# Optimization experiments

Measured on AMD Instinct MI355X. Metric: run time of the kernel, lower is better.

## Reference

```python
import jax, jax.numpy as jnp
import numpy as np

T, D, E, K = 16384, 2048, 128, 8

def setup_inputs() -> dict:
    key = jax.random.key(0)
    k1, k2 = jax.random.split(key)
    hidden_states = jax.random.normal(k1, (T, D), dtype=jnp.float32)
    weight = jax.random.normal(k2, (E, D), dtype=jnp.float32) * 0.02
    return {"hidden_states": hidden_states, "weight": weight}

def reference(hidden_states, weight):
    # (T, D) @ (D, E) -> (T, E) router logits
    x = hidden_states.reshape(-1, weight.shape[1])
    logits = jnp.einsum('td,ed->te', x, weight)
    # softmax in float32 over experts
    router_logits = jax.nn.softmax(logits.astype(jnp.float32), axis=-1)
    # top-k selection + renormalization so selected weights sum to 1
    router_weights, router_indices = jax.lax.top_k(router_logits, K)
    router_weights = router_weights / jnp.sum(router_weights, axis=-1, keepdims=True)
    return (router_logits, router_weights, router_indices)
```

## Files before the change

### kernel.cpp

```cpp
#include <hip/hip_runtime.h>
#include <math.h>


constexpr int T = 16384;
constexpr int D = 2048;
constexpr int E = 128;
constexpr int K = 8;

constexpr int BM = 32;
constexpr int NS = 5;
constexpr int NB = D / 64;

typedef int i32x4 __attribute__((ext_vector_type(4)));

#define MFI8(A, B, C) C = __builtin_amdgcn_mfma_i32_16x16x64_i8(A, B, C, 0, 0, 0)

__device__ __forceinline__ void slice5(float x, float c, float ic, int out[NS]) {
    float r = x;
#pragma unroll
    for (int s = 0; s < NS; ++s) {
        float q = rintf(r * c);
        out[s] = (int)q;
        r = fmaf(q, -ic, r);
        c *= 128.f;
        ic *= (1.f / 128.f);
    }
}

__global__ __launch_bounds__(256)
void w_slice(const float* __restrict__ W, signed char* __restrict__ Ws)
{
    const int e  = blockIdx.x >> 1;
    const int k0 = ((blockIdx.x & 1) << 10) | (threadIdx.x << 2);
    float4 v = *(const float4*)(W + (size_t)e * D + k0);
    int b0[NS], b1[NS], b2[NS], b3[NS];
    slice5(v.x, 512.f, 1.f / 512.f, b0);
    slice5(v.y, 512.f, 1.f / 512.f, b1);
    slice5(v.z, 512.f, 1.f / 512.f, b2);
    slice5(v.w, 512.f, 1.f / 512.f, b3);
#pragma unroll
    for (int s = 0; s < NS; ++s) {
        unsigned lo = __builtin_amdgcn_perm((unsigned)b1[s], (unsigned)b0[s], 0x00000400u);
        unsigned hi = __builtin_amdgcn_perm((unsigned)b3[s], (unsigned)b2[s], 0x00000400u);
        unsigned pk = __builtin_amdgcn_perm(hi, lo, 0x05040100u);
        *(int*)(Ws + (size_t)s * E * D + (size_t)e * D + k0) = (int)pk;
    }
}

__global__ __launch_bounds__(512, 4)
void router_fused(const float* __restrict__ X,
                  const signed char* __restrict__ Ws,
                  float* __restrict__ out)
{
    __shared__ __align__(16) signed char As[2][NS][2][4][16][16];
    __shared__ double Ld[BM][E];

    const int tid = threadIdx.x;
    const long t0 = (long)blockIdx.x * BM;

    const int ar = tid >> 4;
    const int ac = (tid & 15) << 2;
    const float* Xp = X + (t0 + ar) * (long)D + ac;

    const int l  = tid & 63;
    const int wv = tid >> 6;
    const int er = l & 15;
    const int kg = l >> 4;

    const signed char* Wp = Ws + (size_t)(wv * 16 + er) * D + (size_t)kg * 16;

    i32x4 p00 = {}, p01 = {}, p02 = {}, p03 = {}, p04 = {};
    i32x4 p10 = {}, p11 = {}, p12 = {}, p13 = {}, p14 = {};

    auto stage = [&](const float4& v, int buf) {
        int q0[NS], q1[NS], q2[NS], q3[NS];
        slice5(v.x, 16.f, 1.f / 16.f, q0);
        slice5(v.y, 16.f, 1.f / 16.f, q1);
        slice5(v.z, 16.f, 1.f / 16.f, q2);
        slice5(v.w, 16.f, 1.f / 16.f, q3);
        int* dst = (int*)&As[buf][0][ar >> 4][ac >> 4][ar & 15][ac & 15];
#pragma unroll
        for (int s = 0; s < NS; ++s) {
            unsigned lo = __builtin_amdgcn_perm((unsigned)q1[s], (unsigned)q0[s], 0x00000400u);
            unsigned hi = __builtin_amdgcn_perm((unsigned)q3[s], (unsigned)q2[s], 0x00000400u);
            unsigned pk = __builtin_amdgcn_perm(hi, lo, 0x05040100u);
            dst[s * 512] = (int)pk;
        }
    };

    auto tileStep = [&](int buf, int tl,
                        const i32x4& b0, const i32x4& b1, const i32x4& b2,
                        const i32x4& b3, const i32x4& b4,
                        i32x4& d0, i32x4& d1, i32x4& d2, i32x4& d3, i32x4& d4) {
        const signed char* ap = &As[buf][0][tl][0][0][0] + l * 16;
        i32x4 a0 = *(const i32x4*)(ap);
        i32x4 a1 = *(const i32x4*)(ap + 2048);
        i32x4 a2 = *(const i32x4*)(ap + 4096);
        i32x4 a3 = *(const i32x4*)(ap + 6144);
        i32x4 a4 = *(const i32x4*)(ap + 8192);
        MFI8(a0, b0, d0);
        MFI8(a0, b1, d1); MFI8(a1, b0, d1);
        MFI8(a0, b2, d2); MFI8(a1, b1, d2); MFI8(a2, b0, d2);
        MFI8(a0, b3, d3); MFI8(a1, b2, d3); MFI8(a2, b1, d3); MFI8(a3, b0, d3);
        MFI8(a0, b4, d4); MFI8(a1, b3, d4); MFI8(a2, b2, d4); MFI8(a3, b1, d4);
        MFI8(a4, b0, d4);
    };

    float4 xv = *(const float4*)(Xp);
    stage(xv, 0);
    xv = *(const float4*)(Xp + 64);
    __syncthreads();

    for (int p = 0; p < NB; ++p) {
        const int cur = p & 1;
        const long kb = (long)p * 64;

        i32x4 b0 = *(const i32x4*)(Wp + 0UL * E * D + kb);
        i32x4 b1 = *(const i32x4*)(Wp + 1UL * E * D + kb);
        i32x4 b2 = *(const i32x4*)(Wp + 2UL * E * D + kb);
        i32x4 b3 = *(const i32x4*)(Wp + 3UL * E * D + kb);
        i32x4 b4 = *(const i32x4*)(Wp + 4UL * E * D + kb);

        if (p < NB - 1) stage(xv, cur ^ 1);
        if (p < NB - 2) xv = *(const float4*)(Xp + (p + 2) * 64);

        tileStep(cur, 0, b0, b1, b2, b3, b4, p00, p01, p02, p03, p04);
        tileStep(cur, 1, b0, b1, b2, b3, b4, p10, p11, p12, p13, p14);

        __syncthreads();
    }

#pragma unroll
    for (int r = 0; r < 4; ++r) {
        const int row0 = kg * 4 + r;
        const int col  = wv * 16 + er;
        Ld[row0][col]      = (double)p00[r] * 0x1p-13 + (double)p01[r] * 0x1p-20
                           + (double)p02[r] * 0x1p-27 + (double)p03[r] * 0x1p-34
                           + (double)p04[r] * 0x1p-41;
        Ld[row0 + 16][col] = (double)p10[r] * 0x1p-13 + (double)p11[r] * 0x1p-20
                           + (double)p12[r] * 0x1p-27 + (double)p13[r] * 0x1p-34
                           + (double)p14[r] * 0x1p-41;
    }
    __syncthreads();

    float* outL  = out;
    float* outWt = out + (long)T * E;
    float* outId = outWt + (long)T * K;
    const int tx = tid & 15;
    const int tt = tid >> 4;
    const long t = t0 + tt;

    double acc[8];
#pragma unroll
    for (int j = 0; j < 8; ++j) acc[j] = Ld[tt][(tx << 3) + j];

    double m = acc[0];
#pragma unroll
    for (int j = 1; j < 8; ++j) m = fmax(m, acc[j]);
#pragma unroll
    for (int mask = 1; mask <= 8; mask <<= 1)
        m = fmax(m, __shfl_xor(m, mask, 64));

    float e[8]; float s = 0.f;
#pragma unroll
    for (int j = 0; j < 8; ++j) { e[j] = __expf((float)(acc[j] - m)); s += e[j]; }
#pragma unroll
    for (int mask = 1; mask <= 8; mask <<= 1)
        s += __shfl_xor(s, mask, 64);
    const float inv = 1.f / s;

    float4 st0 = {e[0] * inv, e[1] * inv, e[2] * inv, e[3] * inv};
    float4 st1 = {e[4] * inv, e[5] * inv, e[6] * inv, e[7] * inv};
    *(float4*)&outL[t * E + (tx << 3)]     = st0;
    *(float4*)&outL[t * E + (tx << 3) + 4] = st1;

    double v[8];
#pragma unroll
    for (int j = 0; j < 8; ++j) v[j] = acc[j];

    float pk[K]; int ik[K]; float tsum = 0.f;
#pragma unroll
    for (int r = 0; r < K; ++r) {
        double bv = -1.0e300; int bi = 0x7fffffff;
#pragma unroll
        for (int j = 0; j < 8; ++j) {
            const int idx = (tx << 3) + j;
            const bool better = (v[j] > bv) || (v[j] == bv && idx < bi);
            bv = better ? v[j] : bv;
            bi = better ? idx : bi;
        }
#pragma unroll
        for (int mask = 1; mask <= 8; mask <<= 1) {
            const double ov = __shfl_xor(bv, mask, 64);
            const int    oi = __shfl_xor(bi, mask, 64);
            const bool better = (ov > bv) || (ov == bv && oi < bi);
            bv = better ? ov : bv;
            bi = better ? oi : bi;
        }
        const float pw = __expf((float)(bv - m)) * inv;
        pk[r] = pw; ik[r] = bi; tsum += pw;
        const bool own  = ((bi >> 3) == tx);
        const int  slot = bi & 7;
#pragma unroll
        for (int j = 0; j < 8; ++j)
            v[j] = (own && j == slot) ? -1.0e300 : v[j];
    }

    if (tx == 0) {
        const float rinv = 1.f / tsum;
#pragma unroll
        for (int r = 0; r < K; ++r) {
            outWt[t * K + r] = pk[r] * rinv;
            outId[t * K + r] = (float)ik[r];
        }
    }
}

extern "C" void kernel_launch(void* const* d_in, const int* in_sizes, int n_in,
                              void* d_out, int out_size, void* d_ws, size_t ws_size,
                              hipStream_t stream)
{
    const float* X = (const float*)d_in[0];
    const float* W = (const float*)d_in[1];
    float* out = (float*)d_out;
    signed char* Ws = (signed char*)d_ws;

    w_slice<<<dim3(E * 2), dim3(256), 0, stream>>>(W, Ws);
    router_fused<<<dim3(T / BM), dim3(512), 0, stream>>>(X, Ws, out);
}
```

Baseline: 266.8 us.

## Halve token tile and give each wave two expert tiles with reused A fragments

Shrinks the per-block token tile from 32 to 16 rows and the block from 512 to 256 threads. Each of the four waves now covers 32 experts (two 16-wide tiles), loading twice as many W slice fragments per step while reading each A fragment from LDS once for both expert tiles. The MFMA sequence is reordered so consecutive instructions go to independent accumulators and is wrapped in s_setprio. The aim is to cut LDS traffic per MFMA, avoid back-to-back dependent MFMAs, and raise block count, but W global/L2 loads per token double and register pressure rises.

```diff
diff --git a/kernel.cpp b/kernel.cpp
--- a/kernel.cpp
+++ b/kernel.cpp
@@ -7,7 +7,7 @@
 constexpr int E = 128;
 constexpr int K = 8;
 
-constexpr int BM = 32;
+constexpr int BM = 16;
 constexpr int NS = 5;
 constexpr int NB = D / 64;
 
@@ -47,12 +47,12 @@
     }
 }
 
-__global__ __launch_bounds__(512, 4)
+__global__ __launch_bounds__(256, 4)
 void router_fused(const float* __restrict__ X,
                   const signed char* __restrict__ Ws,
                   float* __restrict__ out)
 {
-    __shared__ __align__(16) signed char As[2][NS][2][4][16][16];
+    __shared__ __align__(16) signed char As[2][NS][4][16][16];
     __shared__ double Ld[BM][E];
 
     const int tid = threadIdx.x;
@@ -67,7 +67,8 @@
     const int er = l & 15;
     const int kg = l >> 4;
 
-    const signed char* Wp = Ws + (size_t)(wv * 16 + er) * D + (size_t)kg * 16;
+    const signed char* Wp0 = Ws + (size_t)(wv * 32 + er) * D + (size_t)kg * 16;
+    const signed char* Wp1 = Wp0 + (size_t)16 * D;
 
     i32x4 p00 = {}, p01 = {}, p02 = {}, p03 = {}, p04 = {};
     i32x4 p10 = {}, p11 = {}, p12 = {}, p13 = {}, p14 = {};
@@ -78,32 +79,14 @@
         slice5(v.y, 16.f, 1.f / 16.f, q1);
         slice5(v.z, 16.f, 1.f / 16.f, q2);
         slice5(v.w, 16.f, 1.f / 16.f, q3);
-        int* dst = (int*)&As[buf][0][ar >> 4][ac >> 4][ar & 15][ac & 15];
+        int* dst = (int*)&As[buf][0][ac >> 4][ar][ac & 15];
 #pragma unroll
         for (int s = 0; s < NS; ++s) {
             unsigned lo = __builtin_amdgcn_perm((unsigned)q1[s], (unsigned)q0[s], 0x00000400u);
             unsigned hi = __builtin_amdgcn_perm((unsigned)q3[s], (unsigned)q2[s], 0x00000400u);
             unsigned pk = __builtin_amdgcn_perm(hi, lo, 0x05040100u);
-            dst[s * 512] = (int)pk;
-        }
-    };
-
-    auto tileStep = [&](int buf, int tl,
-                        const i32x4& b0, const i32x4& b1, const i32x4& b2,
-                        const i32x4& b3, const i32x4& b4,
-                        i32x4& d0, i32x4& d1, i32x4& d2, i32x4& d3, i32x4& d4) {
-        const signed char* ap = &As[buf][0][tl][0][0][0] + l * 16;
-        i32x4 a0 = *(const i32x4*)(ap);
-        i32x4 a1 = *(const i32x4*)(ap + 2048);
-        i32x4 a2 = *(const i32x4*)(ap + 4096);
-        i32x4 a3 = *(const i32x4*)(ap + 6144);
-        i32x4 a4 = *(const i32x4*)(ap + 8192);
-        MFI8(a0, b0, d0);
-        MFI8(a0, b1, d1); MFI8(a1, b0, d1);
-        MFI8(a0, b2, d2); MFI8(a1, b1, d2); MFI8(a2, b0, d2);
-        MFI8(a0, b3, d3); MFI8(a1, b2, d3); MFI8(a2, b1, d3); MFI8(a3, b0, d3);
-        MFI8(a0, b4, d4); MFI8(a1, b3, d4); MFI8(a2, b2, d4); MFI8(a3, b1, d4);
-        MFI8(a4, b0, d4);
+            dst[s * 256] = (int)pk;
+        }
     };
 
     float4 xv = *(const float4*)(Xp);
@@ -115,31 +98,57 @@
         const int cur = p & 1;
         const long kb = (long)p * 64;
 
-        i32x4 b0 = *(const i32x4*)(Wp + 0UL * E * D + kb);
-        i32x4 b1 = *(const i32x4*)(Wp + 1UL * E * D + kb);
-        i32x4 b2 = *(const i32x4*)(Wp + 2UL * E * D + kb);
-        i32x4 b3 = *(const i32x4*)(Wp + 3UL * E * D + kb);
-        i32x4 b4 = *(const i32x4*)(Wp + 4UL * E * D + kb);
+        i32x4 b0 = *(const i32x4*)(Wp0 + 0UL * E * D + kb);
+        i32x4 b1 = *(const i32x4*)(Wp0 + 1UL * E * D + kb);
+        i32x4 b2 = *(const i32x4*)(Wp0 + 2UL * E * D + kb);
+        i32x4 b3 = *(const i32x4*)(Wp0 + 3UL * E * D + kb);
+        i32x4 b4 = *(const i32x4*)(Wp0 + 4UL * E * D + kb);
+        i32x4 c0 = *(const i32x4*)(Wp1 + 0UL * E * D + kb);
+        i32x4 c1 = *(const i32x4*)(Wp1 + 1UL * E * D + kb);
+        i32x4 c2 = *(const i32x4*)(Wp1 + 2UL * E * D + kb);
+        i32x4 c3 = *(const i32x4*)(Wp1 + 3UL * E * D + kb);
+        i32x4 c4 = *(const i32x4*)(Wp1 + 4UL * E * D + kb);
 
         if (p < NB - 1) stage(xv, cur ^ 1);
         if (p < NB - 2) xv = *(const float4*)(Xp + (p + 2) * 64);
 
-        tileStep(cur, 0, b0, b1, b2, b3, b4, p00, p01, p02, p03, p04);
-        tileStep(cur, 1, b0, b1, b2, b3, b4, p10, p11, p12, p13, p14);
+        const signed char* ap = &As[cur][0][0][0][0] + l * 16;
+        __builtin_amdgcn_s_setprio(1);
+        i32x4 a;
+        a = *(const i32x4*)(ap);
+        MFI8(a, b0, p00); MFI8(a, c0, p10);
+        MFI8(a, b1, p01); MFI8(a, c1, p11);
+        MFI8(a, b2, p02); MFI8(a, c2, p12);
+        MFI8(a, b3, p03); MFI8(a, c3, p13);
+        MFI8(a, b4, p04); MFI8(a, c4, p14);
+        a = *(const i32x4*)(ap + 1024);
+        MFI8(a, b0, p01); MFI8(a, c0, p11);
+        MFI8(a, b1, p02); MFI8(a, c1, p12);
+        MFI8(a, b2, p03); MFI8(a, c2, p13);
+        MFI8(a, b3, p04); MFI8(a, c3, p14);
+        a = *(const i32x4*)(ap + 2048);
+        MFI8(a, b0, p02); MFI8(a, c0, p12);
+        MFI8(a, b1, p03); MFI8(a, c1, p13);
+        MFI8(a, b2, p04); MFI8(a, c2, p14);
+        a = *(const i32x4*)(ap + 3072);
+        MFI8(a, b0, p03); MFI8(a, c0, p13);
+        MFI8(a, b1, p04); MFI8(a, c1, p14);
+        a = *(const i32x4*)(ap + 4096);
+        MFI8(a, b0, p04); MFI8(a, c0, p14);
+        __builtin_amdgcn_s_setprio(0);
 
         __syncthreads();
     }
 
 #pragma unroll
     for (int r = 0; r < 4; ++r) {
-        const int row0 = kg * 4 + r;
-        const int col  = wv * 16 + er;
-        Ld[row0][col]      = (double)p00[r] * 0x1p-13 + (double)p01[r] * 0x1p-20
-                           + (double)p02[r] * 0x1p-27 + (double)p03[r] * 0x1p-34
-                           + (double)p04[r] * 0x1p-41;
-        Ld[row0 + 16][col] = (double)p10[r] * 0x1p-13 + (double)p11[r] * 0x1p-20
-                           + (double)p12[r] * 0x1p-27 + (double)p13[r] * 0x1p-34
-                           + (double)p14[r] * 0x1p-41;
+        const int row = kg * 4 + r;
+        Ld[row][wv * 32 + er]      = (double)p00[r] * 0x1p-13 + (double)p01[r] * 0x1p-20
+                                   + (double)p02[r] * 0x1p-27 + (double)p03[r] * 0x1p-34
+                                   + (double)p04[r] * 0x1p-41;
+        Ld[row][wv * 32 + 16 + er] = (double)p10[r] * 0x1p-13 + (double)p11[r] * 0x1p-20
+                                   + (double)p12[r] * 0x1p-27 + (double)p13[r] * 0x1p-34
+                                   + (double)p14[r] * 0x1p-41;
     }
     __syncthreads();
 
@@ -226,5 +235,5 @@
     signed char* Ws = (signed char*)d_ws;
 
     w_slice<<<dim3(E * 2), dim3(256), 0, stream>>>(W, Ws);
-    router_fused<<<dim3(T / BM), dim3(512), 0, stream>>>(X, Ws, out);
-}
+    router_fused<<<dim3(T / BM), dim3(256), 0, stream>>>(X, Ws, out);
+}
```

Result: slower. 327.9 us (+22.9%).

## Process two K-chunks per barrier with swizzled LDS and interleaved MFMA order

Applied to the files above, without the earlier changes.

Doubles the K extent handled per loop iteration, from 64 to 128, so the number of __syncthreads barriers is halved and ten W fragments are loaded per iteration. The LDS A-tile layout gains an XOR-like rotation swizzle on the row slot, meant to reduce bank conflicts on the 16-byte fragment reads. The MFMA sequence is reordered to alternate between the two row tiles, reducing back-to-back dependent accumulations. The cost is a doubled LDS footprint and more live registers, which may lower occupancy.

```diff
diff --git a/kernel.cpp b/kernel.cpp
--- a/kernel.cpp
+++ b/kernel.cpp
@@ -7,9 +7,9 @@
 constexpr int E = 128;
 constexpr int K = 8;
 
-constexpr int BM = 32;
-constexpr int NS = 5;
-constexpr int NB = D / 64;
+constexpr int BM  = 32;
+constexpr int NS  = 5;
+constexpr int NB2 = D / 128;
 
 typedef int i32x4 __attribute__((ext_vector_type(4)));
 
@@ -52,7 +52,7 @@
                   const signed char* __restrict__ Ws,
                   float* __restrict__ out)
 {
-    __shared__ __align__(16) signed char As[2][NS][2][4][16][16];
+    __shared__ __align__(16) signed char As[2][2][NS][2][4][16][16];
     __shared__ double Ld[BM][E];
 
     const int tid = threadIdx.x;
@@ -67,18 +67,26 @@
     const int er = l & 15;
     const int kg = l >> 4;
 
-    const signed char* Wp = Ws + (size_t)(wv * 16 + er) * D + (size_t)kg * 16;
-
-    i32x4 p00 = {}, p01 = {}, p02 = {}, p03 = {}, p04 = {};
-    i32x4 p10 = {}, p11 = {}, p12 = {}, p13 = {}, p14 = {};
-
-    auto stage = [&](const float4& v, int buf) {
+    const size_t wbase = (size_t)(wv * 16 + er) * D + (size_t)kg * 16;
+    const signed char* Wq0 = Ws + 0UL * E * D + wbase;
+    const signed char* Wq1 = Ws + 1UL * E * D + wbase;
+    const signed char* Wq2 = Ws + 2UL * E * D + wbase;
+    const signed char* Wq3 = Ws + 3UL * E * D + wbase;
+    const signed char* Wq4 = Ws + 4UL * E * D + wbase;
+
+    const int loff = kg * 256 + (((er + (kg << 2)) & 15) << 4);
+
+    i32x4 e0 = {}, e1 = {}, e2 = {}, e3 = {}, e4 = {};
+    i32x4 f0 = {}, f1 = {}, f2 = {}, f3 = {}, f4 = {};
+
+    auto stage = [&](const float4& v, int buf, int chn) {
         int q0[NS], q1[NS], q2[NS], q3[NS];
         slice5(v.x, 16.f, 1.f / 16.f, q0);
         slice5(v.y, 16.f, 1.f / 16.f, q1);
         slice5(v.z, 16.f, 1.f / 16.f, q2);
         slice5(v.w, 16.f, 1.f / 16.f, q3);
-        int* dst = (int*)&As[buf][0][ar >> 4][ac >> 4][ar & 15][ac & 15];
+        const int slot = ((ar & 15) + ((ac >> 4) << 2)) & 15;
+        int* dst = (int*)&As[buf][chn][0][ar >> 4][ac >> 4][slot][ac & 15];
 #pragma unroll
         for (int s = 0; s < NS; ++s) {
             unsigned lo = __builtin_amdgcn_perm((unsigned)q1[s], (unsigned)q0[s], 0x00000400u);
@@ -88,58 +96,80 @@
         }
     };
 
-    auto tileStep = [&](int buf, int tl,
-                        const i32x4& b0, const i32x4& b1, const i32x4& b2,
-                        const i32x4& b3, const i32x4& b4,
-                        i32x4& d0, i32x4& d1, i32x4& d2, i32x4& d3, i32x4& d4) {
-        const signed char* ap = &As[buf][0][tl][0][0][0] + l * 16;
-        i32x4 a0 = *(const i32x4*)(ap);
-        i32x4 a1 = *(const i32x4*)(ap + 2048);
-        i32x4 a2 = *(const i32x4*)(ap + 4096);
-        i32x4 a3 = *(const i32x4*)(ap + 6144);
-        i32x4 a4 = *(const i32x4*)(ap + 8192);
-        MFI8(a0, b0, d0);
-        MFI8(a0, b1, d1); MFI8(a1, b0, d1);
-        MFI8(a0, b2, d2); MFI8(a1, b1, d2); MFI8(a2, b0, d2);
-        MFI8(a0, b3, d3); MFI8(a1, b2, d3); MFI8(a2, b1, d3); MFI8(a3, b0, d3);
-        MFI8(a0, b4, d4); MFI8(a1, b3, d4); MFI8(a2, b2, d4); MFI8(a3, b1, d4);
-        MFI8(a4, b0, d4);
+    auto chunkMM = [&](const signed char* ap,
+                       const i32x4& b0, const i32x4& b1, const i32x4& b2,
+                       const i32x4& b3, const i32x4& b4) {
+        i32x4 at0, at1;
+        at0 = *(const i32x4*)(ap);           at1 = *(const i32x4*)(ap + 1024);
+        MFI8(at0, b0, e0); MFI8(at0, b1, e1); MFI8(at0, b2, e2); MFI8(at0, b3, e3); MFI8(at0, b4, e4);
+        MFI8(at1, b0, f0); MFI8(at1, b1, f1); MFI8(at1, b2, f2); MFI8(at1, b3, f3); MFI8(at1, b4, f4);
+        at0 = *(const i32x4*)(ap + 2048);    at1 = *(const i32x4*)(ap + 3072);
+        MFI8(at0, b0, e1); MFI8(at0, b1, e2); MFI8(at0, b2, e3); MFI8(at0, b3, e4);
+        MFI8(at1, b0, f1); MFI8(at1, b1, f2); MFI8(at1, b2, f3); MFI8(at1, b3, f4);
+        at0 = *(const i32x4*)(ap + 4096);    at1 = *(const i32x4*)(ap + 5120);
+        MFI8(at0, b0, e2); MFI8(at0, b1, e3); MFI8(at0, b2, e4);
+        MFI8(at1, b0, f2); MFI8(at1, b1, f3); MFI8(at1, b2, f4);
+        at0 = *(const i32x4*)(ap + 6144);    at1 = *(const i32x4*)(ap + 7168);
+        MFI8(at0, b0, e3); MFI8(at0, b1, e4);
+        MFI8(at1, b0, f3); MFI8(at1, b1, f4);
+        at0 = *(const i32x4*)(ap + 8192);    at1 = *(const i32x4*)(ap + 9216);
+        MFI8(at0, b0, e4);
+        MFI8(at1, b0, f4);
     };
 
-    float4 xv = *(const float4*)(Xp);
-    stage(xv, 0);
-    xv = *(const float4*)(Xp + 64);
-    __syncthreads();
-
-    for (int p = 0; p < NB; ++p) {
+    float4 xv0, xv1;
+    {
+        float4 x0 = *(const float4*)(Xp);
+        float4 x1 = *(const float4*)(Xp + 64);
+        stage(x0, 0, 0);
+        stage(x1, 0, 1);
+        xv0 = *(const float4*)(Xp + 128);
+        xv1 = *(const float4*)(Xp + 192);
+        __syncthreads();
+    }
+
+    for (int p = 0; p < NB2; ++p) {
         const int cur = p & 1;
-        const long kb = (long)p * 64;
-
-        i32x4 b0 = *(const i32x4*)(Wp + 0UL * E * D + kb);
-        i32x4 b1 = *(const i32x4*)(Wp + 1UL * E * D + kb);
-        i32x4 b2 = *(const i32x4*)(Wp + 2UL * E * D + kb);
-        i32x4 b3 = *(const i32x4*)(Wp + 3UL * E * D + kb);
-        i32x4 b4 = *(const i32x4*)(Wp + 4UL * E * D + kb);
-
-        if (p < NB - 1) stage(xv, cur ^ 1);
-        if (p < NB - 2) xv = *(const float4*)(Xp + (p + 2) * 64);
-
-        tileStep(cur, 0, b0, b1, b2, b3, b4, p00, p01, p02, p03, p04);
-        tileStep(cur, 1, b0, b1, b2, b3, b4, p10, p11, p12, p13, p14);
+        const long kb = (long)p * 128;
+
+        i32x4 b00 = *(const i32x4*)(Wq0 + kb);
+        i32x4 b01 = *(const i32x4*)(Wq1 + kb);
+        i32x4 b02 = *(const i32x4*)(Wq2 + kb);
+        i32x4 b03 = *(const i32x4*)(Wq3 + kb);
+        i32x4 b04 = *(const i32x4*)(Wq4 + kb);
+        i32x4 b10 = *(const i32x4*)(Wq0 + kb + 64);
+        i32x4 b11 = *(const i32x4*)(Wq1 + kb + 64);
+        i32x4 b12 = *(const i32x4*)(Wq2 + kb + 64);
+        i32x4 b13 = *(const i32x4*)(Wq3 + kb + 64);
+        i32x4 b14 = *(const i32x4*)(Wq4 + kb + 64);
+
+        if (p < NB2 - 1) {
+            stage(xv0, cur ^ 1, 0);
+            stage(xv1, cur ^ 1, 1);
+        }
+        if (p < NB2 - 2) {
+            xv0 = *(const float4*)(Xp + (p + 2) * 128);
+            xv1 = *(const float4*)(Xp + (p + 2) * 128 + 64);
+        }
+
+        const signed char* ap =
+            (const signed char*)&As[cur][0][0][0][0][0][0] + loff;
+        chunkMM(ap,         b00, b01, b02, b03, b04);
+        chunkMM(ap + 10240, b10, b11, b12, b13, b14);
 
         __syncthreads();
     }
 
 #pragma unroll
     for (int r = 0; r < 4; ++r) {
-        const int row0 = kg * 4 + r;
-        const int col  = wv * 16 + er;
-        Ld[row0][col]      = (double)p00[r] * 0x1p-13 + (double)p01[r] * 0x1p-20
-                           + (double)p02[r] * 0x1p-27 + (double)p03[r] * 0x1p-34
-                           + (double)p04[r] * 0x1p-41;
-        Ld[row0 + 16][col] = (double)p10[r] * 0x1p-13 + (double)p11[r] * 0x1p-20
-                           + (double)p12[r] * 0x1p-27 + (double)p13[r] * 0x1p-34
-                           + (double)p14[r] * 0x1p-41;
+        const int row = kg * 4 + r;
+        const int col = wv * 16 + er;
+        Ld[row][col]      = (double)e0[r] * 0x1p-13 + (double)e1[r] * 0x1p-20
+                          + (double)e2[r] * 0x1p-27 + (double)e3[r] * 0x1p-34
+                          + (double)e4[r] * 0x1p-41;
+        Ld[row + 16][col] = (double)f0[r] * 0x1p-13 + (double)f1[r] * 0x1p-20
+                          + (double)f2[r] * 0x1p-27 + (double)f3[r] * 0x1p-34
+                          + (double)f4[r] * 0x1p-41;
     }
     __syncthreads();
 
```

Result: faster. 252.6 us (-5.3%).
